# Optimization experiments

Hardware: AMD Instinct MI355X
Metric: run time of the kernel (lower is better)

## Reference

```python
import jax, jax.numpy as jnp
import numpy as np

V, E, H, B, S = 32000, 256, 512, 64, 2048


def lstm_step(x, h, c, w_ih, w_hh, b_ih, b_hh):
    # single-timestep LSTM cell, PyTorch gate order (i, f, g, o)
    g = x @ w_ih.T + h @ w_hh.T + b_ih + b_hh  # [B, 4H]
    i, f, gg, o = jnp.split(g, 4, axis=-1)
    i = jax.nn.sigmoid(i)
    f = jax.nn.sigmoid(f)
    o = jax.nn.sigmoid(o)
    gg = jnp.tanh(gg)
    c2 = f * c + i * gg
    h2 = o * jnp.tanh(c2)
    return h2, c2


def setup_inputs() -> dict:
    key = jax.random.key(0)
    ks = jax.random.split(key, 20)
    sc = 0.02
    return {
        "x": jax.random.randint(ks[0], (B,), 0, V),
        "hidden_state_decoder": jax.random.normal(ks[1], (B, H), jnp.float32),
        "hidden_state_encoder": jax.random.normal(ks[2], (B, S, H), jnp.float32),
        "hidden_state": jax.random.normal(ks[3], (1, B, H), jnp.float32),
        "cell_state": jax.random.normal(ks[4], (1, B, H), jnp.float32),
        "emb": jax.random.normal(ks[5], (V, E), jnp.float32) * sc,
        "w_ih1": jax.random.normal(ks[6], (4 * H, E + H), jnp.float32) * sc,
        "w_hh1": jax.random.normal(ks[7], (4 * H, H), jnp.float32) * sc,
        "b_ih1": jnp.zeros((4 * H,), jnp.float32),
        "b_hh1": jnp.zeros((4 * H,), jnp.float32),
        "w_ih": jax.random.normal(ks[8], (3, 4 * H, H), jnp.float32) * sc,  # lstm2..4
        "w_hh": jax.random.normal(ks[9], (3, 4 * H, H), jnp.float32) * sc,
        "b_ih": jnp.zeros((3, 4 * H), jnp.float32),
        "b_hh": jnp.zeros((3, 4 * H), jnp.float32),
        "fc_w": jax.random.normal(ks[10], (V, H), jnp.float32) * sc,
        "fc_b": jnp.zeros((V,), jnp.float32),
    }


def reference(x, hidden_state_decoder, hidden_state_encoder, hidden_state, cell_state,
              emb, w_ih1, w_hh1, b_ih1, b_hh1, w_ih, w_hh, b_ih, b_hh, fc_w, fc_b):
    # embedding gather: [B, E]
    xe = emb[x]
    # dot-product attention (Luong): scores [B, S]
    scores = jnp.einsum('bd,bsd->bs', hidden_state_decoder, hidden_state_encoder)
    attn = jax.nn.softmax(scores, axis=-1)
    ctx = jnp.einsum('bs,bsd->bd', attn, hidden_state_encoder)  # [B, H]
    inp = jnp.concatenate([xe, ctx], axis=-1)  # [B, E+H]
    # lstm1 with provided initial state
    h, c = lstm_step(inp, hidden_state[0], cell_state[0], w_ih1, w_hh1, b_ih1, b_hh1)
    z = h
    zeros = jnp.zeros_like(h)
    # lstm2..4 with zero initial states (PyTorch default)
    for l in range(3):
        h, c = lstm_step(z, zeros, zeros, w_ih[l], w_hh[l], b_ih[l], b_hh[l])
        z = h
    logits = z @ fc_w.T + fc_b  # [B, V]
    logits = logits[:, None, :]  # [B, 1, V]
    return logits, h[None], c[None]
```

## Files before the change

### kernel.cpp

```cpp
#include <hip/hip_runtime.h>
#include <cstdint>
#include <cstddef>

constexpr int B = 64, S = 2048, H = 512, E = 256, V = 32000;
constexpr int NCHUNK = 32;

using bf16x8 = __attribute__((ext_vector_type(8))) short;
using f32x4  = __attribute__((ext_vector_type(4))) float;

static __device__ __forceinline__ unsigned short f2bf(float f) {
    unsigned u = __float_as_uint(f);
    u = u + 0x7fffu + ((u >> 16) & 1u);
    return (unsigned short)(u >> 16);
}
static __device__ __forceinline__ float bf2f(unsigned short h) {
    return __uint_as_float(((unsigned)h) << 16);
}

__global__ __launch_bounds__(256) void attn_part_kernel(
    const float* __restrict__ hd, const float* __restrict__ enc,
    float* __restrict__ m_part, float* __restrict__ l_part,
    float* __restrict__ acc_part)
{
    int b = blockIdx.x >> 3;
    int wave = threadIdx.x >> 6, lane = threadIdx.x & 63;
    int chunk = ((blockIdx.x & 7) << 2) + wave;
    int s0 = chunk * 64;

    const float4* hv = (const float4*)(hd + (size_t)b * H);
    float4 h0 = hv[lane], h1 = hv[64 + lane];
    const float4* ev = (const float4*)(enc + (size_t)b * S * H) + (size_t)s0 * (H / 4);

    float m = -1e30f, l = 0.f;
    float4 a0 = make_float4(0.f, 0.f, 0.f, 0.f);
    float4 a1 = make_float4(0.f, 0.f, 0.f, 0.f);
    float4 e0 = ev[lane], e1 = ev[64 + lane];

    auto process = [&](const float4& pe0, const float4& pe1) {
        float p = pe0.x * h0.x + pe0.y * h0.y + pe0.z * h0.z + pe0.w * h0.w
                + pe1.x * h1.x + pe1.y * h1.y + pe1.z * h1.z + pe1.w * h1.w;
#pragma unroll
        for (int off = 32; off; off >>= 1) p += __shfl_xor(p, off, 64);
        if (p <= m) {
            float w = __expf(p - m);
            l += w;
            a0.x += w * pe0.x; a0.y += w * pe0.y; a0.z += w * pe0.z; a0.w += w * pe0.w;
            a1.x += w * pe1.x; a1.y += w * pe1.y; a1.z += w * pe1.z; a1.w += w * pe1.w;
        } else {
            float sc = __expf(m - p);
            m = p;
            l = l * sc + 1.f;
            a0.x = a0.x * sc + pe0.x; a0.y = a0.y * sc + pe0.y;
            a0.z = a0.z * sc + pe0.z; a0.w = a0.w * sc + pe0.w;
            a1.x = a1.x * sc + pe1.x; a1.y = a1.y * sc + pe1.y;
            a1.z = a1.z * sc + pe1.z; a1.w = a1.w * sc + pe1.w;
        }
    };

    for (int s = 0; s < 63; ++s) {
        const float4* r = ev + (size_t)(s + 1) * (H / 4);
        float4 n0 = r[lane], n1 = r[64 + lane];
        process(e0, e1);
        e0 = n0; e1 = n1;
    }
    process(e0, e1);

    int base = b * NCHUNK + chunk;
    if (lane == 0) { m_part[base] = m; l_part[base] = l; }
    float4* ap = (float4*)(acc_part + (size_t)base * H);
    ap[lane] = a0; ap[64 + lane] = a1;
}

__global__ __launch_bounds__(256) void combine_kernel(
    const float* __restrict__ m_part, const float* __restrict__ l_part,
    const float* __restrict__ acc_part, const int* __restrict__ x,
    const float* __restrict__ emb, const float* __restrict__ h0,
    float* __restrict__ inp_t)
{
    int b = blockIdx.x, t = threadIdx.x;
    float M = -1e30f;
    for (int i = 0; i < NCHUNK; ++i) M = fmaxf(M, m_part[b * NCHUNK + i]);
    float L = 0.f;
    for (int i = 0; i < NCHUNK; ++i)
        L += l_part[b * NCHUNK + i] * __expf(m_part[b * NCHUNK + i] - M);
    float invL = 1.f / L;

    for (int d = t; d < H; d += 256) {
        float s = 0.f;
        for (int i = 0; i < NCHUNK; ++i)
            s += __expf(m_part[b * NCHUNK + i] - M) *
                 acc_part[((size_t)(b * NCHUNK + i)) * H + d];
        inp_t[(E + d) * B + b] = s * invL;
    }
    inp_t[t * B + b] = emb[(size_t)x[b] * E + t];
    for (int d = t; d < H; d += 256)
        inp_t[(E + H + d) * B + b] = h0[b * H + d];
}

__global__ __launch_bounds__(256) void lstm_fused_kernel(
    const float* __restrict__ A1, int lda1, int k1len,
    const float* __restrict__ A2, int lda2, int KT,
    const float* __restrict__ X,
    const float* __restrict__ b_ih, const float* __restrict__ b_hh,
    const float* __restrict__ c_prev,
    float* __restrict__ h_t, float* __restrict__ out_h, float* __restrict__ out_c)
{
    __shared__ float sm[4 * 32 * 20 + 4 * 32 * 64];
    float (*As)[32][20] = (float(*)[32][20])sm;
    float (*Xs)[32][64] = (float(*)[32][64])(sm + 4 * 32 * 20);
    float (*Ps)[16][64] = (float(*)[16][64])(sm + 4 * 32 * 20);

    const int t = threadIdx.x;
    const int j0 = blockIdx.x * 4;
    const int QK = KT >> 2;
    const int nIter = QK >> 5;
    const int kq = t >> 6, r = t & 63, ty = r >> 4, tx = r & 15;

    float acc[4][4];
#pragma unroll
    for (int i = 0; i < 4; ++i)
#pragma unroll
        for (int j = 0; j < 4; ++j) acc[i][j] = 0.f;

    for (int it = 0; it < nIter; ++it) {
#pragma unroll
        for (int q = 0; q < 2; ++q) {
            int p = t + q * 256;
            int il = p >> 5, c = p & 31;
            int akq = c >> 3, k4 = (c & 7) * 4;
            int gk = akq * QK + it * 32 + k4;
            int grow = j0 + (il & 3) + 512 * (il >> 2);
            const float* src = (gk < k1len)
                ? A1 + (size_t)grow * lda1 + gk
                : A2 + (size_t)grow * lda2 + (gk - k1len);
            float4 v = *(const float4*)src;
            As[akq][k4 + 0][il] = v.x; As[akq][k4 + 1][il] = v.y;
            As[akq][k4 + 2][il] = v.z; As[akq][k4 + 3][il] = v.w;
        }
#pragma unroll
        for (int q = 0; q < 8; ++q) {
            int p = t + q * 256;
            int kk_all = p >> 4, col = (p & 15) * 4;
            int xkq = kk_all >> 5, kk = kk_all & 31;
            int gk = xkq * QK + it * 32 + kk;
            *(float4*)&Xs[xkq][kk][col] = *(const float4*)&X[(size_t)gk * 64 + col];
        }
        __syncthreads();

#pragma unroll 8
        for (int kk = 0; kk < 32; ++kk) {
            float4 av = *(const float4*)&As[kq][kk][ty * 4];
            float4 xv = *(const float4*)&Xs[kq][kk][tx * 4];
            float aa[4] = {av.x, av.y, av.z, av.w};
            float xx[4] = {xv.x, xv.y, xv.z, xv.w};
#pragma unroll
            for (int i = 0; i < 4; ++i)
#pragma unroll
                for (int j = 0; j < 4; ++j) acc[i][j] += aa[i] * xx[j];
        }
        __syncthreads();
    }

#pragma unroll
    for (int i = 0; i < 4; ++i)
        *(float4*)&Ps[kq][ty * 4 + i][tx * 4] =
            make_float4(acc[i][0], acc[i][1], acc[i][2], acc[i][3]);
    __syncthreads();

    for (int idx = t; idx < 16 * 64; idx += 256) {
        int row = idx >> 6, b = idx & 63;
        Ps[0][row][b] = Ps[0][row][b] + Ps[1][row][b] + Ps[2][row][b] + Ps[3][row][b];
    }
    __syncthreads();

    {
        int jj = t >> 6, b = t & 63;
        int j = j0 + jj;
        float gi = Ps[0][jj][b]      + b_ih[j]        + b_hh[j];
        float gf = Ps[0][4 + jj][b]  + b_ih[j + 512]  + b_hh[j + 512];
        float gg = Ps[0][8 + jj][b]  + b_ih[j + 1024] + b_hh[j + 1024];
        float go = Ps[0][12 + jj][b] + b_ih[j + 1536] + b_hh[j + 1536];
        float iv = 1.f / (1.f + __expf(-gi));
        float fv = 1.f / (1.f + __expf(-gf));
        float gv = tanhf(gg);
        float ov = 1.f / (1.f + __expf(-go));
        float cp = c_prev ? c_prev[b * H + j] : 0.f;
        float c2 = fv * cp + iv * gv;
        float hv = ov * tanhf(c2);
        h_t[j * B + b] = hv;
        if (out_h) { out_h[b * H + j] = hv; out_c[b * H + j] = c2; }
    }
}

__global__ __launch_bounds__(256) void fc_mfma_kernel(
    const float* __restrict__ A, const float* __restrict__ X,
    float* __restrict__ outp, const float* __restrict__ bias)
{
    __shared__ unsigned short zb[64 * 512];

    const int t = threadIdx.x;

    {
        int b = t & 63;
        int kq0 = (t >> 6) * 4;
        for (int q = 0; q < 32; ++q) {
            int k = kq0 + q * 16;
            float f0 = X[(size_t)(k + 0) * 64 + b];
            float f1 = X[(size_t)(k + 1) * 64 + b];
            float f2 = X[(size_t)(k + 2) * 64 + b];
            float f3 = X[(size_t)(k + 3) * 64 + b];
            unsigned lo = (unsigned)f2bf(f0) | ((unsigned)f2bf(f1) << 16);
            unsigned hi = (unsigned)f2bf(f2) | ((unsigned)f2bf(f3) << 16);
            int byte = (b << 10) + (k << 1);
            byte ^= (b & 7) << 4;
            *(uint2*)((char*)zb + byte) = make_uint2(lo, hi);
        }
    }
    __syncthreads();

    const int wv = t >> 6;
    const int l  = t & 63;
    const int row = l & 15, kq = l >> 4;
    const int m0 = blockIdx.x * 64 + wv * 16;
    const float* Arow = A + (size_t)(m0 + row) * 512 + kq * 8;

    f32x4 acc[4];
#pragma unroll
    for (int bt = 0; bt < 4; ++bt) acc[bt] = (f32x4){0.f, 0.f, 0.f, 0.f};

    for (int k0 = 0; k0 < 512; k0 += 32) {
        float4 wa = *(const float4*)(Arow + k0);
        float4 wb = *(const float4*)(Arow + k0 + 4);
        float wf[8] = {wa.x, wa.y, wa.z, wa.w, wb.x, wb.y, wb.z, wb.w};
        bf16x8 whi, wlo;
#pragma unroll
        for (int j = 0; j < 8; ++j) {
            unsigned short h = f2bf(wf[j]);
            whi[j] = (short)h;
            wlo[j] = (short)f2bf(wf[j] - bf2f(h));
        }
#pragma unroll
        for (int bt = 0; bt < 4; ++bt) {
            int b = bt * 16 + row;
            int byte = (b << 10) + ((k0 + kq * 8) << 1);
            byte ^= (b & 7) << 4;
            bf16x8 zf = *(const bf16x8*)((const char*)zb + byte);
            acc[bt] = __builtin_amdgcn_mfma_f32_16x16x32_bf16(whi, zf, acc[bt], 0, 0, 0);
            acc[bt] = __builtin_amdgcn_mfma_f32_16x16x32_bf16(wlo, zf, acc[bt], 0, 0, 0);
        }
    }

    int v0 = m0 + kq * 4;
    float4 bv = *(const float4*)&bias[v0];
#pragma unroll
    for (int bt = 0; bt < 4; ++bt) {
        int b = bt * 16 + row;
        float4 o;
        o.x = acc[bt][0] + bv.x;
        o.y = acc[bt][1] + bv.y;
        o.z = acc[bt][2] + bv.z;
        o.w = acc[bt][3] + bv.w;
        *(float4*)&outp[(size_t)b * V + v0] = o;
    }
}

extern "C" void kernel_launch(void* const* d_in, const int* in_sizes, int n_in,
                              void* d_out, int out_size, void* d_ws, size_t ws_size,
                              hipStream_t stream)
{
    const int*   x     = (const int*)d_in[0];
    const float* hdec  = (const float*)d_in[1];
    const float* enc   = (const float*)d_in[2];
    const float* h0    = (const float*)d_in[3];
    const float* c0    = (const float*)d_in[4];
    const float* emb   = (const float*)d_in[5];
    const float* w_ih1 = (const float*)d_in[6];
    const float* w_hh1 = (const float*)d_in[7];
    const float* b_ih1 = (const float*)d_in[8];
    const float* b_hh1 = (const float*)d_in[9];
    const float* w_ih  = (const float*)d_in[10];
    const float* b_ih  = (const float*)d_in[12];
    const float* b_hh  = (const float*)d_in[13];
    const float* fc_w  = (const float*)d_in[14];
    const float* fc_b  = (const float*)d_in[15];

    float* out = (float*)d_out;
    float* ws  = (float*)d_ws;

    float* m_part   = ws;
    float* l_part   = ws + 2048;
    float* acc_part = ws + 4096;
    float* inp_t    = acc_part + (size_t)B * NCHUNK * H;
    float* zA       = inp_t + 1280 * B;
    float* zB       = zA + H * B;

    float* out_h = out + (size_t)B * V;
    float* out_c = out_h + (size_t)B * H;

    attn_part_kernel<<<512, 256, 0, stream>>>(hdec, enc, m_part, l_part, acc_part);
    combine_kernel<<<64, 256, 0, stream>>>(m_part, l_part, acc_part, x, emb, h0, inp_t);

    lstm_fused_kernel<<<128, 256, 0, stream>>>(
        w_ih1, 768, 768, w_hh1, 512, 1280, inp_t,
        b_ih1, b_hh1, c0, zA, nullptr, nullptr);

    lstm_fused_kernel<<<128, 256, 0, stream>>>(
        w_ih + 0 * (size_t)2048 * H, 512, 512, nullptr, 0, 512, zA,
        b_ih + 0 * 2048, b_hh + 0 * 2048, nullptr, zB, nullptr, nullptr);
    lstm_fused_kernel<<<128, 256, 0, stream>>>(
        w_ih + 1 * (size_t)2048 * H, 512, 512, nullptr, 0, 512, zB,
        b_ih + 1 * 2048, b_hh + 1 * 2048, nullptr, zA, nullptr, nullptr);
    lstm_fused_kernel<<<128, 256, 0, stream>>>(
        w_ih + 2 * (size_t)2048 * H, 512, 512, nullptr, 0, 512, zA,
        b_ih + 2 * 2048, b_hh + 2 * 2048, nullptr, zB, out_h, out_c);

    fc_mfma_kernel<<<500, 256, 0, stream>>>(fc_w, zB, out, fc_b);
}
```

Measured before the change: 152.0 us.

## Emit bf16 activations from last LSTM and stream FC weights via LDS double buffer

The last LSTM layer now also writes its hidden output as row-major bf16, so the FC kernel no longer converts and stages the whole 64x512 activation matrix in shared memory per block. It reads activation fragments straight from global memory instead. FC weights are staged in a double-buffered LDS tile with coalesced loads. The hi/lo bf16 split becomes truncation with bit masks rather than round-to-nearest. This trades a large per-block prologue for a sync every K step and repeated global reads of activations, which are likely L2-hot, and the truncation slightly changes how the hi/lo parts are rounded.

Result: no change. 152.2 us (+0.2%).

```diff
diff --git a/kernel.cpp b/kernel.cpp
--- a/kernel.cpp
+++ b/kernel.cpp
@@ -12,9 +12,6 @@
     unsigned u = __float_as_uint(f);
     u = u + 0x7fffu + ((u >> 16) & 1u);
     return (unsigned short)(u >> 16);
-}
-static __device__ __forceinline__ float bf2f(unsigned short h) {
-    return __uint_as_float(((unsigned)h) << 16);
 }
 
 __global__ __launch_bounds__(256) void attn_part_kernel(
@@ -103,7 +100,8 @@
     const float* __restrict__ X,
     const float* __restrict__ b_ih, const float* __restrict__ b_hh,
     const float* __restrict__ c_prev,
-    float* __restrict__ h_t, float* __restrict__ out_h, float* __restrict__ out_c)
+    float* __restrict__ h_t, float* __restrict__ out_h, float* __restrict__ out_c,
+    unsigned short* __restrict__ zbf)
 {
     __shared__ float sm[4 * 32 * 20 + 4 * 32 * 64];
     float (*As)[32][20] = (float(*)[32][20])sm;
@@ -189,65 +187,78 @@
         float hv = ov * tanhf(c2);
         h_t[j * B + b] = hv;
         if (out_h) { out_h[b * H + j] = hv; out_c[b * H + j] = c2; }
+        if (zbf)   { zbf[(size_t)b * H + j] = f2bf(hv); }
     }
 }
 
 __global__ __launch_bounds__(256) void fc_mfma_kernel(
-    const float* __restrict__ A, const float* __restrict__ X,
+    const float* __restrict__ A, const unsigned short* __restrict__ zbf,
     float* __restrict__ outp, const float* __restrict__ bias)
 {
-    __shared__ unsigned short zb[64 * 512];
+    __shared__ float Wt[2][64][36];
 
     const int t = threadIdx.x;
+    const int wv  = t >> 6;
+    const int l   = t & 63;
+    const int row = l & 15;
+    const int kq  = l >> 4;
+    const int rl  = wv * 16 + row;
+    const int mblk = blockIdx.x * 64;
+    const int m0   = mblk + wv * 16;
+
+    const int st_r = t >> 2, st_c = t & 3;
+    const float* Asrc = A + (size_t)(mblk + st_r) * 512 + st_c * 8;
+
+    f32x4 acc[4];
+#pragma unroll
+    for (int bt = 0; bt < 4; ++bt) acc[bt] = (f32x4){0.f, 0.f, 0.f, 0.f};
 
     {
-        int b = t & 63;
-        int kq0 = (t >> 6) * 4;
-        for (int q = 0; q < 32; ++q) {
-            int k = kq0 + q * 16;
-            float f0 = X[(size_t)(k + 0) * 64 + b];
-            float f1 = X[(size_t)(k + 1) * 64 + b];
-            float f2 = X[(size_t)(k + 2) * 64 + b];
-            float f3 = X[(size_t)(k + 3) * 64 + b];
-            unsigned lo = (unsigned)f2bf(f0) | ((unsigned)f2bf(f1) << 16);
-            unsigned hi = (unsigned)f2bf(f2) | ((unsigned)f2bf(f3) << 16);
-            int byte = (b << 10) + (k << 1);
-            byte ^= (b & 7) << 4;
-            *(uint2*)((char*)zb + byte) = make_uint2(lo, hi);
-        }
+        float4 v0 = *(const float4*)(Asrc + 0);
+        float4 v1 = *(const float4*)(Asrc + 4);
+        *(float4*)&Wt[0][st_r][st_c * 8]     = v0;
+        *(float4*)&Wt[0][st_r][st_c * 8 + 4] = v1;
     }
     __syncthreads();
 
-    const int wv = t >> 6;
-    const int l  = t & 63;
-    const int row = l & 15, kq = l >> 4;
-    const int m0 = blockIdx.x * 64 + wv * 16;
-    const float* Arow = A + (size_t)(m0 + row) * 512 + kq * 8;
-
-    f32x4 acc[4];
-#pragma unroll
-    for (int bt = 0; bt < 4; ++bt) acc[bt] = (f32x4){0.f, 0.f, 0.f, 0.f};
-
-    for (int k0 = 0; k0 < 512; k0 += 32) {
-        float4 wa = *(const float4*)(Arow + k0);
-        float4 wb = *(const float4*)(Arow + k0 + 4);
+    for (int s = 0; s < 16; ++s) {
+        const int buf = s & 1;
+        if (s < 15) {
+            const float* src = Asrc + (s + 1) * 32;
+            float4 v0 = *(const float4*)(src + 0);
+            float4 v1 = *(const float4*)(src + 4);
+            *(float4*)&Wt[buf ^ 1][st_r][st_c * 8]     = v0;
+            *(float4*)&Wt[buf ^ 1][st_r][st_c * 8 + 4] = v1;
+        }
+
+        const float* wrow = &Wt[buf][rl][kq * 8];
+        float4 wa = *(const float4*)wrow;
+        float4 wb = *(const float4*)(wrow + 4);
         float wf[8] = {wa.x, wa.y, wa.z, wa.w, wb.x, wb.y, wb.z, wb.w};
-        bf16x8 whi, wlo;
-#pragma unroll
-        for (int j = 0; j < 8; ++j) {
-            unsigned short h = f2bf(wf[j]);
-            whi[j] = (short)h;
-            wlo[j] = (short)f2bf(wf[j] - bf2f(h));
-        }
+
+        unsigned hd[4], ld[4];
+#pragma unroll
+        for (int p = 0; p < 4; ++p) {
+            unsigned u0 = __float_as_uint(wf[2 * p]);
+            unsigned u1 = __float_as_uint(wf[2 * p + 1]);
+            hd[p] = (u0 >> 16) | (u1 & 0xffff0000u);
+            float r0 = wf[2 * p]     - __uint_as_float(u0 & 0xffff0000u);
+            float r1 = wf[2 * p + 1] - __uint_as_float(u1 & 0xffff0000u);
+            ld[p] = (__float_as_uint(r0) >> 16) | (__float_as_uint(r1) & 0xffff0000u);
+        }
+        union { uint4 u; bf16x8 v; } cvh, cvl;
+        cvh.u = make_uint4(hd[0], hd[1], hd[2], hd[3]);
+        cvl.u = make_uint4(ld[0], ld[1], ld[2], ld[3]);
+
+        const int kgl = s * 32 + kq * 8;
 #pragma unroll
         for (int bt = 0; bt < 4; ++bt) {
             int b = bt * 16 + row;
-            int byte = (b << 10) + ((k0 + kq * 8) << 1);
-            byte ^= (b & 7) << 4;
-            bf16x8 zf = *(const bf16x8*)((const char*)zb + byte);
-            acc[bt] = __builtin_amdgcn_mfma_f32_16x16x32_bf16(whi, zf, acc[bt], 0, 0, 0);
-            acc[bt] = __builtin_amdgcn_mfma_f32_16x16x32_bf16(wlo, zf, acc[bt], 0, 0, 0);
-        }
+            bf16x8 zf = *(const bf16x8*)(zbf + (size_t)b * 512 + kgl);
+            acc[bt] = __builtin_amdgcn_mfma_f32_16x16x32_bf16(cvh.v, zf, acc[bt], 0, 0, 0);
+            acc[bt] = __builtin_amdgcn_mfma_f32_16x16x32_bf16(cvl.v, zf, acc[bt], 0, 0, 0);
+        }
+        __syncthreads();
     }
 
     int v0 = m0 + kq * 4;
@@ -293,6 +304,7 @@
     float* inp_t    = acc_part + (size_t)B * NCHUNK * H;
     float* zA       = inp_t + 1280 * B;
     float* zB       = zA + H * B;
+    unsigned short* zbf = (unsigned short*)(zB + H * B);
 
     float* out_h = out + (size_t)B * V;
     float* out_c = out_h + (size_t)B * H;
@@ -302,17 +314,17 @@
 
     lstm_fused_kernel<<<128, 256, 0, stream>>>(
         w_ih1, 768, 768, w_hh1, 512, 1280, inp_t,
-        b_ih1, b_hh1, c0, zA, nullptr, nullptr);
+        b_ih1, b_hh1, c0, zA, nullptr, nullptr, nullptr);
 
     lstm_fused_kernel<<<128, 256, 0, stream>>>(
         w_ih + 0 * (size_t)2048 * H, 512, 512, nullptr, 0, 512, zA,
-        b_ih + 0 * 2048, b_hh + 0 * 2048, nullptr, zB, nullptr, nullptr);
+        b_ih + 0 * 2048, b_hh + 0 * 2048, nullptr, zB, nullptr, nullptr, nullptr);
     lstm_fused_kernel<<<128, 256, 0, stream>>>(
         w_ih + 1 * (size_t)2048 * H, 512, 512, nullptr, 0, 512, zB,
-        b_ih + 1 * 2048, b_hh + 1 * 2048, nullptr, zA, nullptr, nullptr);
+        b_ih + 1 * 2048, b_hh + 1 * 2048, nullptr, zA, nullptr, nullptr, nullptr);
     lstm_fused_kernel<<<128, 256, 0, stream>>>(
         w_ih + 2 * (size_t)2048 * H, 512, 512, nullptr, 0, 512, zA,
-        b_ih + 2 * 2048, b_hh + 2 * 2048, nullptr, zB, out_h, out_c);
-
-    fc_mfma_kernel<<<500, 256, 0, stream>>>(fc_w, zB, out, fc_b);
-}
+        b_ih + 2 * 2048, b_hh + 2 * 2048, nullptr, zB, out_h, out_c, zbf);
+
+    fc_mfma_kernel<<<500, 256, 0, stream>>>(fc_w, zbf, out, fc_b);
+}
```
